# Optimization experiments

Hardware: AMD Instinct MI355X
Metric: run time of the kernel (lower is better)

## Reference

```python
import jax, jax.numpy as jnp
import numpy as np
from jax import lax

# dims
B, S, NF, E = 128, 256, 32, 4
D, H = 256, 4
DI = 2 * D            # mLSTM inner (up-projection) dim
DHM, DHS = DI // H, D // H
K = 4                 # causal conv kernel size
FF = 352              # gated FFN dim (~4/3 * D, sLSTM block post-FFN)
NE, NP = 100, 6


def _ln(x, g, b, eps=1e-5):
    mu = x.mean(-1, keepdims=True)
    v = x.var(-1, keepdims=True)
    return (x - mu) / jnp.sqrt(v + eps) * g + b


def _cconv(x, w, b):
    # depthwise causal conv1d: x [B,S,C], w [K,C], b [C]
    k = w.shape[0]
    xp = jnp.pad(x, ((0, 0), (k - 1, 0), (0, 0)))
    y = lax.conv_general_dilated(xp, w[:, None, :], (1,), 'VALID',
                                 dimension_numbers=('NWC', 'WIO', 'NWC'),
                                 feature_group_count=x.shape[-1])
    return y + b


def _headnorm(x, g, b, eps=1e-6):
    # per-head group norm: normalize over last (head-dim) axis
    mu = x.mean(-1, keepdims=True)
    v = x.var(-1, keepdims=True)
    return (x - mu) / jnp.sqrt(v + eps) * g + b


def _forward(emb_esn, emb_prof, W_in, b_in,
             m_ln_g, m_ln_b, m_Wup, m_bup, m_convW, m_convb,
             m_Wq, m_bq, m_Wk, m_bk, m_Wv, m_bv,
             m_Wi, m_bi, m_Wf, m_bf, m_skip, m_ng, m_nb, m_Wdown, m_bdown,
             s_ln_g, s_ln_b, s_convW, s_convb,
             s_Wi, s_bi, s_Wf, s_bf, s_Wz, s_bz, s_Wo, s_bo,
             s_Ri, s_Rf, s_Rz, s_Ro, s_ng, s_nb,
             f_ln_g, f_ln_b, f_Wup, f_bup, f_Wdown, f_bdown,
             h_W1, h_b1, h_W2, h_b2,
             x_sens, x_esn, x_prof):
    Bx, Sx = x_sens.shape[0], x_sens.shape[1]
    ve = jnp.broadcast_to(emb_esn[x_esn][:, None, :], (Bx, Sx, E))
    vp = jnp.broadcast_to(emb_prof[x_prof][:, None, :], (Bx, Sx, E))
    x = jnp.concatenate([x_sens, ve, vp], -1) @ W_in + b_in  # [B,S,D]

    # ---------------- block 0: mLSTM (parallel stabilized matrix memory) ----
    xn = _ln(x, m_ln_g, m_ln_b)
    up = xn @ m_Wup + m_bup
    xm, zg = jnp.split(up, 2, axis=-1)              # [B,S,DI] each
    a = jax.nn.silu(_cconv(xm, m_convW, m_convb))   # causal conv + SiLU
    q = a @ m_Wq + m_bq
    k = a @ m_Wk + m_bk
    v = xm @ m_Wv + m_bv
    gin = jnp.concatenate([q, k, v], -1)            # [B,S,3*DI]
    ipre = (gin @ m_Wi + m_bi).transpose(0, 2, 1)   # [B,H,S]
    fpre = (gin @ m_Wf + m_bf).transpose(0, 2, 1)

    def heads(t, dh):
        return t.reshape(Bx, Sx, H, dh).transpose(0, 2, 1, 3)
    qh, kh, vh = heads(q, DHM), heads(k, DHM), heads(v, DHM)  # [B,H,S,dh]

    lfg = jax.nn.log_sigmoid(fpre)
    F = jnp.cumsum(lfg, -1)                         # [B,H,S]
    logD = F[:, :, :, None] - F[:, :, None, :] + ipre[:, :, None, :]
    mask = jnp.tril(jnp.ones((Sx, Sx), bool))
    logD = jnp.where(mask, logD, -jnp.inf)
    mstab = logD.max(-1, keepdims=True)             # [B,H,S,1]
    Dm = jnp.exp(logD - mstab)
    scores = jnp.einsum('bhtd,bhsd->bhts', qh, kh) / np.sqrt(DHM).astype(np.float32)
    C = scores * Dm
    nrm = jnp.maximum(jnp.abs(C.sum(-1, keepdims=True)), jnp.exp(-mstab))
    hh = jnp.einsum('bhts,bhsd->bhtd', C, vh) / nrm
    hn = _headnorm(hh, m_ng.reshape(1, H, 1, DHM), m_nb.reshape(1, H, 1, DHM))
    hn = hn.transpose(0, 2, 1, 3).reshape(Bx, Sx, DI)
    hn = hn + m_skip * a                            # learnable skip from conv branch
    x = x + (hn * jax.nn.silu(zg)) @ m_Wdown + m_bdown

    # ---------------- block 1: sLSTM (stabilized scalar recurrent scan) -----
    xn = _ln(x, s_ln_g, s_ln_b)
    ac = jax.nn.silu(_cconv(xn, s_convW, s_convb))
    to_t = lambda t: t.reshape(Bx, Sx, H, DHS).transpose(1, 0, 2, 3)  # [S,B,H,dh]
    it = to_t(ac @ s_Wi + s_bi)
    ft = to_t(ac @ s_Wf + s_bf)
    zt = to_t(xn @ s_Wz + s_bz)
    ot = to_t(xn @ s_Wo + s_bo)

    def step(carry, xs):
        h, c, n, m = carry
        i0, f0, z0, o0 = xs
        ip = i0 + jnp.einsum('bhd,hde->bhe', h, s_Ri)
        fp = f0 + jnp.einsum('bhd,hde->bhe', h, s_Rf)
        zp = jnp.tanh(z0 + jnp.einsum('bhd,hde->bhe', h, s_Rz))
        op = jax.nn.sigmoid(o0 + jnp.einsum('bhd,hde->bhe', h, s_Ro))
        mn = jnp.maximum(fp + m, ip)
        ig = jnp.exp(ip - mn)
        fg = jnp.exp(fp + m - mn)
        c = fg * c + ig * zp
        n = fg * n + ig
        h = op * c / n
        return (h, c, n, mn), h

    init = tuple(jnp.zeros((Bx, H, DHS), x.dtype) for _ in range(4))
    _, hs = lax.scan(step, init, (it, ft, zt, ot))  # hs [S,B,H,dh]
    hs = _headnorm(hs, s_ng.reshape(1, 1, H, DHS), s_nb.reshape(1, 1, H, DHS))
    x = x + hs.transpose(1, 0, 2, 3).reshape(Bx, Sx, D)

    # gated FFN (sLSTM block post-feedforward)
    xn = _ln(x, f_ln_g, f_ln_b)
    g_, u_ = jnp.split(xn @ f_Wup + f_bup, 2, axis=-1)
    x = x + (jax.nn.gelu(g_) * u_) @ f_Wdown + f_bdown

    last = x[:, -1, :]
    return jax.nn.relu(last @ h_W1 + h_b1) @ h_W2 + h_b2


def setup_inputs() -> dict:
    key = jax.random.key(0)
    ks = iter(jax.random.split(key, 64))
    nrm = lambda sh, s=0.02: jax.random.normal(next(ks), sh, jnp.float32) * s
    z = lambda sh: jnp.zeros(sh, jnp.float32)
    o = lambda sh: jnp.ones(sh, jnp.float32)
    return dict(
        x_sens=jax.random.normal(next(ks), (B, S, NF), jnp.float32),
        x_esn=jax.random.randint(next(ks), (B,), 0, NE, jnp.int32),
        x_prof=jax.random.randint(next(ks), (B,), 0, NP, jnp.int32),
        emb_esn=nrm((NE + 1, E)), emb_prof=nrm((NP + 1, E)),
        W_in=nrm((NF + 2 * E, D)), b_in=z((D,)),
        m_ln_g=o((D,)), m_ln_b=z((D,)),
        m_Wup=nrm((D, 2 * DI)), m_bup=z((2 * DI,)),
        m_convW=nrm((K, DI)), m_convb=z((DI,)),
        m_Wq=nrm((DI, DI)), m_bq=z((DI,)),
        m_Wk=nrm((DI, DI)), m_bk=z((DI,)),
        m_Wv=nrm((DI, DI)), m_bv=z((DI,)),
        m_Wi=nrm((3 * DI, H)), m_bi=z((H,)),
        m_Wf=nrm((3 * DI, H)), m_bf=o((H,)),
        m_skip=o((DI,)), m_ng=o((DI,)), m_nb=z((DI,)),
        m_Wdown=nrm((DI, D)), m_bdown=z((D,)),
        s_ln_g=o((D,)), s_ln_b=z((D,)),
        s_convW=nrm((K, D)), s_convb=z((D,)),
        s_Wi=nrm((D, D)), s_bi=z((D,)),
        s_Wf=nrm((D, D)), s_bf=o((D,)),
        s_Wz=nrm((D, D)), s_bz=z((D,)),
        s_Wo=nrm((D, D)), s_bo=z((D,)),
        s_Ri=nrm((H, DHS, DHS)), s_Rf=nrm((H, DHS, DHS)),
        s_Rz=nrm((H, DHS, DHS)), s_Ro=nrm((H, DHS, DHS)),
        s_ng=o((D,)), s_nb=z((D,)),
        f_ln_g=o((D,)), f_ln_b=z((D,)),
        f_Wup=nrm((D, 2 * FF)), f_bup=z((2 * FF,)),
        f_Wdown=nrm((FF, D)), f_bdown=z((D,)),
        h_W1=nrm((D, 64), 0.05), h_b1=z((64,)),
        h_W2=nrm((64, 3), 0.05), h_b2=z((3,)),
    )


def reference(emb_esn, emb_prof, W_in, b_in,
              m_ln_g, m_ln_b, m_Wup, m_bup, m_convW, m_convb,
              m_Wq, m_bq, m_Wk, m_bk, m_Wv, m_bv,
              m_Wi, m_bi, m_Wf, m_bf, m_skip, m_ng, m_nb, m_Wdown, m_bdown,
              s_ln_g, s_ln_b, s_convW, s_convb,
              s_Wi, s_bi, s_Wf, s_bf, s_Wz, s_bz, s_Wo, s_bo,
              s_Ri, s_Rf, s_Rz, s_Ro, s_ng, s_nb,
              f_ln_g, f_ln_b, f_Wup, f_bup, f_Wdown, f_bdown,
              h_W1, h_b1, h_W2, h_b2,
              x_sens, x_esn, x_prof):
    return _forward(emb_esn, emb_prof, W_in, b_in,
                    m_ln_g, m_ln_b, m_Wup, m_bup, m_convW, m_convb,
                    m_Wq, m_bq, m_Wk, m_bk, m_Wv, m_bv,
                    m_Wi, m_bi, m_Wf, m_bf, m_skip, m_ng, m_nb, m_Wdown, m_bdown,
                    s_ln_g, s_ln_b, s_convW, s_convb,
                    s_Wi, s_bi, s_Wf, s_bf, s_Wz, s_bz, s_Wo, s_bo,
                    s_Ri, s_Rf, s_Rz, s_Ro, s_ng, s_nb,
                    f_ln_g, f_ln_b, f_Wup, f_bup, f_Wdown, f_bdown,
                    h_W1, h_b1, h_W2, h_b2,
                    x_sens, x_esn, x_prof)
```

## Files before the change

kernel.cpp:

```cpp
#include <hip/hip_runtime.h>
#include <cstdint>
#include <cstddef>


using u16 = unsigned short;
using u32 = unsigned int;

typedef __attribute__((ext_vector_type(8))) short short8;
typedef __attribute__((ext_vector_type(8))) unsigned short ushort8v;
typedef __attribute__((ext_vector_type(4))) float float4v;

#define DEVINL __device__ __forceinline__

DEVINL float b2f(u16 u){ u32 x = ((u32)u) << 16; return __builtin_bit_cast(float, x); }
DEVINL u16 f2b(float f){
  u32 x = __builtin_bit_cast(u32, f);
  u32 r = x + 0x7FFFu + ((x >> 16) & 1u);
  return (u16)(r >> 16);
}
DEVINL float ldval(float x){ return x; }
DEVINL float ldval(u16 x){ return b2f(x); }
DEVINL void stval(float* p, float v){ *p = v; }
DEVINL void stval(u16* p, float v){ *p = f2b(v); }

DEVINL void lds_barrier(){
  asm volatile("s_waitcnt lgkmcnt(0)" ::: "memory");
  __builtin_amdgcn_sched_barrier(0);
  __builtin_amdgcn_s_barrier();
  __builtin_amdgcn_sched_barrier(0);
}

DEVINL void dpp_sum2(float a, float b, float& oa, float& ob){
  int xa, xb;
  xa = __builtin_amdgcn_update_dpp(0, __builtin_bit_cast(int, a), 0x111, 0xf, 0xf, true);
  xb = __builtin_amdgcn_update_dpp(0, __builtin_bit_cast(int, b), 0x111, 0xf, 0xf, true);
  a += __builtin_bit_cast(float, xa); b += __builtin_bit_cast(float, xb);
  xa = __builtin_amdgcn_update_dpp(0, __builtin_bit_cast(int, a), 0x112, 0xf, 0xf, true);
  xb = __builtin_amdgcn_update_dpp(0, __builtin_bit_cast(int, b), 0x112, 0xf, 0xf, true);
  a += __builtin_bit_cast(float, xa); b += __builtin_bit_cast(float, xb);
  xa = __builtin_amdgcn_update_dpp(0, __builtin_bit_cast(int, a), 0x114, 0xf, 0xf, true);
  xb = __builtin_amdgcn_update_dpp(0, __builtin_bit_cast(int, b), 0x114, 0xf, 0xf, true);
  a += __builtin_bit_cast(float, xa); b += __builtin_bit_cast(float, xb);
  xa = __builtin_amdgcn_update_dpp(0, __builtin_bit_cast(int, a), 0x118, 0xf, 0xf, true);
  xb = __builtin_amdgcn_update_dpp(0, __builtin_bit_cast(int, b), 0x118, 0xf, 0xf, true);
  a += __builtin_bit_cast(float, xa); b += __builtin_bit_cast(float, xb);
  xa = __builtin_amdgcn_update_dpp(0, __builtin_bit_cast(int, a), 0x142, 0xf, 0xf, true);
  xb = __builtin_amdgcn_update_dpp(0, __builtin_bit_cast(int, b), 0x142, 0xf, 0xf, true);
  a += __builtin_bit_cast(float, xa); b += __builtin_bit_cast(float, xb);
  xa = __builtin_amdgcn_update_dpp(0, __builtin_bit_cast(int, a), 0x143, 0xf, 0xf, true);
  xb = __builtin_amdgcn_update_dpp(0, __builtin_bit_cast(int, b), 0x143, 0xf, 0xf, true);
  a += __builtin_bit_cast(float, xa); b += __builtin_bit_cast(float, xb);
  oa = __builtin_bit_cast(float, __builtin_amdgcn_readlane(__builtin_bit_cast(int, a), 63));
  ob = __builtin_bit_cast(float, __builtin_amdgcn_readlane(__builtin_bit_cast(int, b), 63));
}

constexpr int IN_N = 56;
constexpr long long IN_SIZES[IN_N] = {
  1048576, 128, 128, 404, 28, 10240, 256, 256, 256,
  262144, 1024, 2048, 512,
  262144, 512, 262144, 512, 262144, 512,
  6144, 4, 6144, 4,
  512, 512, 512, 131072, 256,
  256, 256, 1024, 256,
  65536, 256, 65536, 256, 65536, 256, 65536, 256,
  16384, 16384, 16384, 16384,
  256, 256,
  256, 256, 180224, 704, 90112, 256,
  16384, 64, 192, 3 };

constexpr bool is_wt_input(int i){
  return i==9 || i==13 || i==15 || i==17 || i==26 || i==32 || i==34 || i==36
      || i==38 || i==48 || i==50;
}

struct CvOff { long long off[IN_N+1]; };
constexpr CvOff make_off(){
  CvOff o{};
  long long a = 0;
  for (int i = 0; i < IN_N; i++){
    o.off[i] = a;
    long long s = IN_SIZES[i];
    if (i == 1 || i == 2 || is_wt_input(i)) s = 0;
    a += s;
  }
  o.off[IN_N] = a;
  return o;
}
constexpr CvOff CVOFF = make_off();
constexpr long long CV_TOTAL = CVOFF.off[IN_N];

constexpr int WT_NW = 11;
constexpr int WTB_IN[WT_NW] = {9, 13, 15, 17, 26, 32, 34, 36, 38, 48, 50};
constexpr int WTB_K[WT_NW]  = {256,512,512,512,512,256,256,256,256,256,352};
constexpr int WTB_N[WT_NW]  = {1024,512,512,512,256,256,256,256,256,704,256};
constexpr long long WTO[WT_NW+1] = {0, 262144, 524288, 786432, 1048576, 1179648,
  1245184, 1310720, 1376256, 1441792, 1622016, 1712128};
constexpr long long WT_ELEMS = WTO[WT_NW];

constexpr long long alignup(long long x){ return ((x + 255) / 256) * 256; }
constexpr long long TOK = 32768;
constexpr long long OFF_FLAG = alignup(CV_TOTAL);
constexpr long long OFF_IP  = OFF_FLAG + 64;
constexpr long long OFF_FP  = OFF_IP  + 131072;
constexpr long long OFF_F   = OFF_FP  + 131072;
constexpr long long OFF_G   = OFF_F   + 131072;
constexpr long long OFF_M   = OFF_G   + 131072;
constexpr long long OFF_X   = OFF_M   + 131072;
constexpr long long OFF_XN  = OFF_X   + TOK*256;
constexpr long long OFF_UP  = OFF_XN  + TOK*128;
constexpr long long OFF_A   = OFF_UP  + TOK*512;
constexpr long long OFF_Q   = OFF_A   + TOK*256;
constexpr long long OFF_K   = OFF_Q   + TOK*256;
constexpr long long OFF_V   = OFF_K   + TOK*256;
constexpr long long OFF_WT  = OFF_V   + TOK*256;
constexpr long long WS_END  = OFF_WT  + WT_ELEMS/2 + 256;


__global__ void detect_kernel(const void* mlng, int* flag){
  if (threadIdx.x == 0){
    u32 u = *(const u32*)mlng;
    *flag = (u == 0x3F803F80u) ? 1 : 0;
  }
}

struct InPtrs { const void* p[IN_N]; };

__global__ __launch_bounds__(256) void convert_kernel(InPtrs ptrs, float* __restrict__ cv,
                                                      const int* __restrict__ flag){
  long long gid = (long long)blockIdx.x * 256 + threadIdx.x;
  if (gid >= CV_TOTAL) return;
  int seg = 0;
#pragma unroll
  for (int i = 1; i < IN_N; i++) seg += (gid >= CVOFF.off[i]) ? 1 : 0;
  long long local = gid - CVOFF.off[seg];
  float v;
  if (*flag) v = b2f(((const u16*)ptrs.p[seg])[local]);
  else       v = ((const float*)ptrs.p[seg])[local];
  cv[gid] = v;
}

__global__ __launch_bounds__(256) void wtrans_kernel(InPtrs ptrs, u16* __restrict__ WTb,
                                                     const int* __restrict__ flag){
  int wz = blockIdx.z;
  int K = WTB_K[wz], N = WTB_N[wz];
  int n0 = blockIdx.x * 32, k0 = blockIdx.y * 32;
  if (n0 >= N || k0 >= K) return;
  const void* W = ptrs.p[WTB_IN[wz]];
  u16* WT = WTb + WTO[wz];
  __shared__ u16 tile[32][34];
  int tx = threadIdx.x & 31, ty = threadIdx.x >> 5;
  bool bf = (*flag != 0);
#pragma unroll
  for (int i = 0; i < 4; i++){
    size_t src = (size_t)(k0 + ty + i*8)*N + n0 + tx;
    tile[ty + i*8][tx] = bf ? ((const u16*)W)[src] : f2b(((const float*)W)[src]);
  }
  __syncthreads();
#pragma unroll
  for (int i = 0; i < 4; i++)
    WT[(size_t)(n0 + ty + i*8)*K + k0 + tx] = tile[tx][ty + i*8];
}

__global__ __launch_bounds__(256) void cat_kernel(const float* __restrict__ xs,
    const int* __restrict__ xe, const int* __restrict__ xp,
    const float* __restrict__ ee, const float* __restrict__ ep,
    float* __restrict__ CAT){
  int gid = blockIdx.x * 256 + threadIdx.x;
  int c = gid % 40; int t = gid / 40; int b = t >> 8;
  float v;
  if (c < 32)      v = xs[(size_t)t*32 + c];
  else if (c < 36) v = ee[xe[b]*4 + (c - 32)];
  else             v = ep[xp[b]*4 + (c - 36)];
  CAT[(size_t)t*40 + c] = v;
}

template<typename TA, typename TC>
__global__ __launch_bounds__(256) void gemm_kernel(
    const TA* __restrict__ A, int lda,
    const float* __restrict__ Wm, const float* __restrict__ bias,
    TC* __restrict__ Cc, int ldc, const float* __restrict__ resid,
    int M, int N, int K)
{
  __shared__ float As[16][68];
  __shared__ float Bs[16][68];
  const int bm = blockIdx.y * 64, bn = blockIdx.x * 64;
  const int tid = threadIdx.x, tx = tid & 15, ty = tid >> 4;
  float acc[4][4] = {};
  for (int k0 = 0; k0 < K; k0 += 16){
#pragma unroll
    for (int i = 0; i < 4; i++){
      int idx = tid + i*256;
      int m = idx >> 4, kq = idx & 15;
      As[kq][m] = (k0 + kq < K) ? ldval(A[(size_t)(bm + m)*lda + k0 + kq]) : 0.f;
      int kk = idx >> 6, n = idx & 63;
      Bs[kk][n] = (k0 + kk < K) ? Wm[(size_t)(k0 + kk)*N + bn + n] : 0.f;
    }
    __syncthreads();
#pragma unroll
    for (int kq = 0; kq < 16; kq++){
      float av[4], bv[4];
#pragma unroll
      for (int i = 0; i < 4; i++) av[i] = As[kq][ty*4 + i];
#pragma unroll
      for (int j = 0; j < 4; j++) bv[j] = Bs[kq][tx*4 + j];
#pragma unroll
      for (int i = 0; i < 4; i++)
#pragma unroll
        for (int j = 0; j < 4; j++) acc[i][j] += av[i]*bv[j];
    }
    __syncthreads();
  }
#pragma unroll
  for (int i = 0; i < 4; i++){
    int m = bm + ty*4 + i;
#pragma unroll
    for (int j = 0; j < 4; j++){
      int n = bn + tx*4 + j;
      float v = acc[i][j] + bias[n];
      if (resid) v += resid[(size_t)m*ldc + n];
      stval(&Cc[(size_t)m*ldc + n], v);
    }
  }
}

template<typename TC>
__global__ __launch_bounds__(256) void gemm_mfma(
    const u16* __restrict__ A, int lda,
    const u16* __restrict__ WT,
    const float* __restrict__ bias,
    TC* __restrict__ Cc, int ldc, const float* __restrict__ resid,
    int N, int K)
{
  __shared__ alignas(16) u16 As[128*40];
  __shared__ alignas(16) u16 Bs[128*40];
  const int bm = blockIdx.y * 128, bn = blockIdx.x * 128;
  const int tid = threadIdx.x;
  const int w = tid >> 6, lane = tid & 63, lm = lane & 15, q = lane >> 4;
  const int wm = w >> 1, wn = w & 1;
  float4v acc[4][4] = {};
  for (int k0 = 0; k0 < K; k0 += 32){
    __syncthreads();
#pragma unroll
    for (int c = tid; c < 512; c += 256){
      int r = c >> 2, ch = c & 3;
      *(uint4*)&As[r*40 + ch*8] = *(const uint4*)&A[(size_t)(bm + r)*lda + k0 + ch*8];
      int n = bn + r;
      uint4 bv = {0u,0u,0u,0u};
      if (n < N) bv = *(const uint4*)&WT[(size_t)n*K + k0 + ch*8];
      *(uint4*)&Bs[r*40 + ch*8] = bv;
    }
    __syncthreads();
    short8 a[4], b[4];
#pragma unroll
    for (int i = 0; i < 4; i++)
      a[i] = *(const short8*)&As[(wm*64 + i*16 + lm)*40 + q*8];
#pragma unroll
    for (int j = 0; j < 4; j++)
      b[j] = *(const short8*)&Bs[(wn*64 + j*16 + lm)*40 + q*8];
#pragma unroll
    for (int i = 0; i < 4; i++)
#pragma unroll
      for (int j = 0; j < 4; j++)
        acc[i][j] = __builtin_amdgcn_mfma_f32_16x16x32_bf16(a[i], b[j], acc[i][j], 0, 0, 0);
  }
#pragma unroll
  for (int i = 0; i < 4; i++){
#pragma unroll
    for (int j = 0; j < 4; j++){
      int col = bn + wn*64 + j*16 + lm;
      if (col < N){
#pragma unroll
        for (int r = 0; r < 4; r++){
          int row = bm + wm*64 + i*16 + q*4 + r;
          float v = acc[i][j][r] + bias[col];
          if (resid) v += resid[(size_t)row*ldc + col];
          stval(&Cc[(size_t)row*ldc + col], v);
        }
      }
    }
  }
}

__global__ __launch_bounds__(256) void ln_kernel(const float* __restrict__ Xin,
    const float* __restrict__ g, const float* __restrict__ b,
    u16* __restrict__ out, float eps){
  int t = blockIdx.x*4 + (threadIdx.x >> 6);
  int e = threadIdx.x & 63;
  float4 v = *(const float4*)&Xin[(size_t)t*256 + e*4];
  float su = v.x + v.y + v.z + v.w;
#pragma unroll
  for (int o = 32; o > 0; o >>= 1) su += __shfl_xor(su, o, 64);
  float mu = su * (1.f/256.f);
  float d0 = v.x - mu, d1 = v.y - mu, d2 = v.z - mu, d3 = v.w - mu;
  float sq = d0*d0 + d1*d1 + d2*d2 + d3*d3;
#pragma unroll
  for (int o = 32; o > 0; o >>= 1) sq += __shfl_xor(sq, o, 64);
  float rstd = rsqrtf(sq * (1.f/256.f) + eps);
  float4 gv = *(const float4*)&g[e*4];
  float4 bv = *(const float4*)&b[e*4];
  ushort4 o4;
  o4.x = f2b(d0*rstd*gv.x + bv.x);
  o4.y = f2b(d1*rstd*gv.y + bv.y);
  o4.z = f2b(d2*rstd*gv.z + bv.z);
  o4.w = f2b(d3*rstd*gv.w + bv.w);
  *(ushort4*)&out[(size_t)t*256 + e*4] = o4;
}

__global__ __launch_bounds__(256) void conv_silu_kernel(const u16* __restrict__ Xc, int ldx, int C,
    const float* __restrict__ w, const float* __restrict__ bias, u16* __restrict__ Y){
  int nc = C >> 3;
  long long gid = (long long)blockIdx.x * 256 + threadIdx.x;
  int c8 = (int)(gid % nc) * 8; long long t = gid / nc;
  int s = (int)(t & 255);
  float acc[8];
#pragma unroll
  for (int i = 0; i < 8; i++) acc[i] = bias[c8 + i];
#pragma unroll
  for (int j = 0; j < 4; j++){
    int so = s - 3 + j;
    if (so >= 0){
      ushort8v xv = *(const ushort8v*)&Xc[(size_t)(t - 3 + j)*ldx + c8];
#pragma unroll
      for (int i = 0; i < 8; i++) acc[i] += b2f(xv[i]) * w[j*C + c8 + i];
    }
  }
  ushort8v o8;
#pragma unroll
  for (int i = 0; i < 8; i++) o8[i] = f2b(acc[i] / (1.f + __expf(-acc[i])));
  *(ushort8v*)&Y[(size_t)t*C + c8] = o8;
}

__global__ __launch_bounds__(256) void gates_kernel(
    const u16* __restrict__ Q, const u16* __restrict__ Kb, const u16* __restrict__ V,
    const float* __restrict__ Wi, const float* __restrict__ bi,
    const float* __restrict__ Wf, const float* __restrict__ bf,
    float* __restrict__ IP, float* __restrict__ FP){
  int t = blockIdx.x; int tid = threadIdx.x;
  int o = tid & 7, seg = tid >> 3;
  int b = t >> 8, s = t & 255;
  int g = o & 3;
  const float* Wg = (o >= 4) ? Wf : Wi;
  float part = 0.f;
#pragma unroll
  for (int i = 0; i < 6; i++){
    int k8 = seg*48 + i*8;
    const u16* src; int off;
    if (k8 < 512){ src = Q; off = k8; }
    else if (k8 < 1024){ src = Kb; off = k8 - 512; }
    else { src = V; off = k8 - 1024; }
    ushort8v gv = *(const ushort8v*)&src[(size_t)t*512 + off];
#pragma unroll
    for (int j = 0; j < 8; j++) part += b2f(gv[j]) * Wg[(k8 + j)*4 + g];
  }
  __shared__ float red[256];
  red[tid] = part; __syncthreads();
  if (tid < 8){
    float tot = 0.f;
    for (int ss = 0; ss < 32; ss++) tot += red[ss*8 + tid];
    int gg = tid & 3;
    if (tid < 4) IP[(b*4 + gg)*256 + s] = tot + bi[gg];
    else         FP[(b*4 + gg)*256 + s] = tot + bf[gg];
  }
}

__global__ __launch_bounds__(256) void fscan_kernel(const float* __restrict__ IP,
    const float* __restrict__ FP, float* __restrict__ Fo, float* __restrict__ Go,
    float* __restrict__ Mo){
  int bh = blockIdx.x; int s = threadIdx.x;
  int idx = bh*256 + s;
  __shared__ float buf[256];
  float fp = FP[idx];
  float lfg = fminf(fp, 0.f) - log1pf(expf(-fabsf(fp)));
  float v = lfg;
  buf[s] = v; __syncthreads();
  for (int off = 1; off < 256; off <<= 1){
    float tv = (s >= off) ? buf[s - off] : 0.f;
    __syncthreads();
    v += tv; buf[s] = v;
    __syncthreads();
  }
  float Fv = v;
  float g = IP[idx] - Fv;
  float mv = g;
  buf[s] = mv; __syncthreads();
  for (int off = 1; off < 256; off <<= 1){
    float tv = (s >= off) ? buf[s - off] : -3.0e38f;
    __syncthreads();
    mv = fmaxf(mv, tv); buf[s] = mv;
    __syncthreads();
  }
  Fo[idx] = Fv; Go[idx] = g; Mo[idx] = mv;
}

__global__ __launch_bounds__(256) void attn_kernel(
    const u16* __restrict__ Q, const u16* __restrict__ Kb, const u16* __restrict__ V,
    const float* __restrict__ G, const float* __restrict__ Mx, const float* __restrict__ F,
    const u16* __restrict__ Ab, const u16* __restrict__ UPb,
    const float* __restrict__ ng, const float* __restrict__ nb,
    const float* __restrict__ skip, u16* __restrict__ Yb)
{
  int bh = blockIdx.y, b = bh >> 2, h = bh & 3;
  int tt = blockIdx.x, t0 = tt * 64;
  int tid = threadIdx.x;
  int w = tid >> 6, lane = tid & 63, lm = lane & 15, q = lane >> 4;
  int gbase = bh * 256;

  __shared__ alignas(16) u16 Qs[64*136];
  __shared__ alignas(16) u16 Ks[64*136];
  __shared__ alignas(16) u16 Vt[128*72];
  __shared__ alignas(16) u16 Ps[64*72];
  __shared__ float rs[64];

#pragma unroll
  for (int c = tid; c < 1024; c += 256){
    int r = c >> 4, ch = c & 15;
    *(uint4*)&Qs[r*136 + ch*8] =
      *(const uint4*)&Q[((size_t)(b*256 + t0 + r))*512 + h*128 + ch*8];
  }
  if (tid < 64) rs[tid] = 0.f;

  float mrow[4];
#pragma unroll
  for (int r = 0; r < 4; r++) mrow[r] = Mx[gbase + t0 + w*16 + q*4 + r];

  float4v acc2[8] = {};
  const float scale = 0.08838834764831845f;

  for (int ss = 0; ss <= tt; ss++){
    int s0 = ss * 64;
    __syncthreads();
#pragma unroll
    for (int c = tid; c < 1024; c += 256){
      int r = c >> 4, ch = c & 15;
      *(uint4*)&Ks[r*136 + ch*8] =
        *(const uint4*)&Kb[((size_t)(b*256 + s0 + r))*512 + h*128 + ch*8];
    }
#pragma unroll
    for (int c = tid; c < 1024; c += 256){
      int sl = c & 63, db = c >> 6;
      ushort8v v = *(const ushort8v*)&V[((size_t)(b*256 + s0 + sl))*512 + h*128 + db*8];
#pragma unroll
      for (int j = 0; j < 8; j++) Vt[(db*8 + j)*72 + sl] = v[j];
    }
    __syncthreads();
    float4v sacc[4] = {};
#pragma unroll
    for (int k0 = 0; k0 < 128; k0 += 32){
      short8 a = *(const short8*)&Qs[(w*16 + lm)*136 + k0 + q*8];
#pragma unroll
      for (int j = 0; j < 4; j++){
        short8 bb = *(const short8*)&Ks[(j*16 + lm)*136 + k0 + q*8];
        sacc[j] = __builtin_amdgcn_mfma_f32_16x16x32_bf16(a, bb, sacc[j], 0, 0, 0);
      }
    }
    float rp[4] = {0.f, 0.f, 0.f, 0.f};
#pragma unroll
    for (int j = 0; j < 4; j++){
      int scol = s0 + j*16 + lm;
      float gq = G[gbase + scol];
#pragma unroll
      for (int r = 0; r < 4; r++){
        int trow = t0 + w*16 + q*4 + r;
        float cval = (scol <= trow) ? sacc[j][r]*scale*__expf(gq - mrow[r]) : 0.f;
        Ps[(w*16 + q*4 + r)*72 + j*16 + lm] = f2b(cval);
        rp[r] += cval;
      }
    }
#pragma unroll
    for (int r = 0; r < 4; r++){
#pragma unroll
      for (int m = 1; m < 16; m <<= 1) rp[r] += __shfl_xor(rp[r], m, 16);
      if (lm == 0) rs[w*16 + q*4 + r] += rp[r];
    }
#pragma unroll
    for (int k0 = 0; k0 < 64; k0 += 32){
      short8 a = *(const short8*)&Ps[(w*16 + lm)*72 + k0 + q*8];
#pragma unroll
      for (int jd = 0; jd < 8; jd++){
        short8 bb = *(const short8*)&Vt[(jd*16 + lm)*72 + k0 + q*8];
        acc2[jd] = __builtin_amdgcn_mfma_f32_16x16x32_bf16(a, bb, acc2[jd], 0, 0, 0);
      }
    }
  }
  __syncthreads();
#pragma unroll
  for (int r = 0; r < 4; r++){
    int rl = w*16 + q*4 + r;
    int t = t0 + rl;
    float Fv = F[gbase + t];
    float nrm = fmaxf(fabsf(rs[rl]), __expf(-(Fv + mrow[r])));
    float inv = 1.f / nrm;
    float vv[8];
    float su = 0.f;
#pragma unroll
    for (int jd = 0; jd < 8; jd++){ vv[jd] = acc2[jd][r]*inv; su += vv[jd]; }
#pragma unroll
    for (int m = 1; m < 16; m <<= 1) su += __shfl_xor(su, m, 16);
    float mu = su * (1.f/128.f);
    float sq = 0.f;
#pragma unroll
    for (int jd = 0; jd < 8; jd++){ vv[jd] -= mu; sq += vv[jd]*vv[jd]; }
#pragma unroll
    for (int m = 1; m < 16; m <<= 1) sq += __shfl_xor(sq, m, 16);
    float rstd = rsqrtf(sq * (1.f/128.f) + 1e-6f);
#pragma unroll
    for (int jd = 0; jd < 8; jd++){
      int c = h*128 + jd*16 + lm;
      float hv = vv[jd]*rstd*ng[c] + nb[c];
      float av = b2f(Ab[(size_t)t*512 + c]);
      float zg = b2f(UPb[(size_t)t*1024 + 512 + c]);
      float sz = zg / (1.f + __expf(-zg));
      Yb[(size_t)t*512 + c] = f2b((hv + skip[c]*av)*sz);
    }
  }
}

__global__ __launch_bounds__(320) void scan_kernel(
    const float* __restrict__ G1, const float* __restrict__ G2,
    const float* __restrict__ Ri, const float* __restrict__ Rf,
    const float* __restrict__ Rz, const float* __restrict__ Ro,
    const float* __restrict__ sng, const float* __restrict__ snb,
    float* __restrict__ Xr){
  int bh = blockIdx.x; int b = bh >> 2, h = bh & 3;
  int e = threadIdx.x & 63;
  int w = threadIdx.x >> 6;
  __shared__ float4 part[2][4][64];
  __shared__ float hbuf[2][64];
  size_t xrow = ((size_t)b*256)*256 + h*64 + e;

  if (w < 4){
    float r0[16], r1[16], r2[16], r3[16];
    const float* Rp0 = Ri + h*4096 + w*1024;
    const float* Rp1 = Rf + h*4096 + w*1024;
    const float* Rp2 = Rz + h*4096 + w*1024;
    const float* Rp3 = Ro + h*4096 + w*1024;
#pragma unroll
    for (int d = 0; d < 16; d++){
      r0[d] = Rp0[d*64 + e];
      r1[d] = Rp1[d*64 + e];
      r2[d] = Rp2[d*64 + e];
      r3[d] = Rp3[d*64 + e];
    }
    const float* Gp = (w < 2) ? G1 : G2;
    size_t grow = ((size_t)b*256)*512 + ((w & 1) ? 256 : 0) + h*64 + e;
    float hS = 0.f, cS = 0.f, nS = 0.f, mS = 0.f;
    float gv = Gp[grow];
    float gn = Gp[grow + 512];
    for (int s = 0; s < 256; s++){
      float gn2 = 0.f;
      if (s < 254) gn2 = Gp[grow + (size_t)(s + 2)*512];
      float ai0 = 0.f, ai1 = 0.f, af0 = 0.f, af1 = 0.f;
      float az0 = 0.f, az1 = 0.f, ao0 = 0.f, ao1 = 0.f;
#pragma unroll
      for (int k = 0; k < 16; k += 2){
        float h0 = __builtin_bit_cast(float,
            __builtin_amdgcn_readlane(__builtin_bit_cast(int, hS), w*16 + k));
        float h1 = __builtin_bit_cast(float,
            __builtin_amdgcn_readlane(__builtin_bit_cast(int, hS), w*16 + k + 1));
        ai0 += h0*r0[k]; ai1 += h1*r0[k+1];
        af0 += h0*r1[k]; af1 += h1*r1[k+1];
        az0 += h0*r2[k]; az1 += h1*r2[k+1];
        ao0 += h0*r3[k]; ao1 += h1*r3[k+1];
      }
      float4 p;
      p.x = ai0 + ai1; p.y = af0 + af1; p.z = az0 + az1; p.w = ao0 + ao1;
      if      (w == 0) p.x += gv;
      else if (w == 1) p.y += gv;
      else if (w == 2) p.z += gv;
      else             p.w += gv;
      part[s & 1][w][e] = p;
      lds_barrier();
      float4 q0 = part[s & 1][0][e];
      float4 q1 = part[s & 1][1][e];
      float4 q2 = part[s & 1][2][e];
      float4 q3 = part[s & 1][3][e];
      float ip = (q0.x + q1.x) + (q2.x + q3.x);
      float fp = (q0.y + q1.y) + (q2.y + q3.y);
      float zr = (q0.z + q1.z) + (q2.z + q3.z);
      float og = (q0.w + q1.w) + (q2.w + q3.w);
      float zp = 1.f - 2.f*__builtin_amdgcn_rcpf(__expf(2.f*zr) + 1.f);
      float op = __builtin_amdgcn_rcpf(1.f + __expf(-og));
      float mn = fmaxf(fp + mS, ip);
      float ig = __expf(ip - mn);
      float fg = __expf(fp + mS - mn);
      cS = fg*cS + ig*zp;
      nS = fg*nS + ig;
      mS = mn;
      hS = op * cS * __builtin_amdgcn_rcpf(nS);
      if (w == 1) hbuf[s & 1][e] = hS;
      gv = gn; gn = gn2;
    }
    lds_barrier();
  } else {
    float gw = sng[h*64 + e], bw = snb[h*64 + e];
    float xp = 0.f, xc = 0.f;
    for (int s = 0; s < 256; s++){
      xc = Xr[xrow + (size_t)s*256];
      lds_barrier();
      if (s > 0){
        float hv = hbuf[(s - 1) & 1][e];
        float su, sq;
        dpp_sum2(hv, hv*hv, su, sq);
        float mu = su * (1.f/64.f);
        float var = fmaxf(sq * (1.f/64.f) - mu*mu, 0.f);
        float nv = (hv - mu) * rsqrtf(var + 1e-6f) * gw + bw;
        Xr[xrow + (size_t)(s - 1)*256] = xp + nv;
      }
      xp = xc;
    }
    lds_barrier();
    float hv = hbuf[1][e];
    float su, sq;
    dpp_sum2(hv, hv*hv, su, sq);
    float mu = su * (1.f/64.f);
    float var = fmaxf(sq * (1.f/64.f) - mu*mu, 0.f);
    float nv = (hv - mu) * rsqrtf(var + 1e-6f) * gw + bw;
    Xr[xrow + (size_t)255*256] = xp + nv;
  }
}

__global__ __launch_bounds__(256) void ffn_act_kernel(const u16* __restrict__ GU,
                                                      u16* __restrict__ P){
  long long gid = (long long)blockIdx.x * 256 + threadIdx.x;
  int j8 = (int)(gid % 44) * 8; long long t = gid / 44;
  ushort8v gv = *(const ushort8v*)&GU[(size_t)t*704 + j8];
  ushort8v uv = *(const ushort8v*)&GU[(size_t)t*704 + 352 + j8];
  ushort8v o8;
#pragma unroll
  for (int i = 0; i < 8; i++){
    float g = b2f(gv[i]);
    float u = b2f(uv[i]);
    float inner = 0.7978845608028654f * (g + 0.044715f*g*g*g);
    float gel = 0.5f * g * (1.f + tanhf(inner));
    o8[i] = f2b(gel * u);
  }
  *(ushort8v*)&P[(size_t)t*352 + j8] = o8;
}

__global__ __launch_bounds__(64) void head_kernel(const float* __restrict__ X,
    const float* __restrict__ W1, const float* __restrict__ b1,
    const float* __restrict__ W2, const float* __restrict__ b2,
    void* out, const int* __restrict__ flag){
  int b = blockIdx.x, j = threadIdx.x;
  __shared__ float L[256];
  __shared__ float H1[64];
  for (int i = j; i < 256; i += 64) L[i] = X[((size_t)(b*256 + 255))*256 + i];
  __syncthreads();
  float acc = b1[j];
  for (int d = 0; d < 256; d++) acc += L[d] * W1[d*64 + j];
  H1[j] = fmaxf(acc, 0.f);
  __syncthreads();
  if (j < 3){
    float o = b2[j];
    for (int k2 = 0; k2 < 64; k2++) o += H1[k2] * W2[k2*3 + j];
    if (*flag) ((u16*)out)[b*3 + j] = f2b(o);
    else       ((float*)out)[b*3 + j] = o;
  }
}

extern "C" void kernel_launch(void* const* d_in, const int* in_sizes, int n_in,
                              void* d_out, int out_size, void* d_ws, size_t ws_size,
                              hipStream_t stream)
{
  if (n_in != IN_N) return;
  for (int i = 0; i < IN_N; i++) if ((long long)in_sizes[i] != IN_SIZES[i]) return;
  if (ws_size < (size_t)WS_END * 4) return;
  if (out_size != 384) return;

  float* ws = (float*)d_ws;
  float* cv = ws;
  auto cvp = [&](int i){ return cv + CVOFF.off[i]; };

  int*   flag = (int*)(ws + OFF_FLAG);
  float* IP   = ws + OFF_IP;
  float* FP   = ws + OFF_FP;
  float* Fb   = ws + OFF_F;
  float* Gb   = ws + OFF_G;
  float* Mb   = ws + OFF_M;
  float* X    = ws + OFF_X;
  u16*   XNb  = (u16*)(ws + OFF_XN);
  u16*   UPb  = (u16*)(ws + OFF_UP);
  u16*   Ab   = (u16*)(ws + OFF_A);
  u16*   Qb   = (u16*)(ws + OFF_Q);
  u16*   Kbb  = (u16*)(ws + OFF_K);
  u16*   Vb   = (u16*)(ws + OFF_V);
  u16*   WTb  = (u16*)(ws + OFF_WT);
  float* CAT = ws + OFF_V;
  u16*   Yb  = Qb;
  u16*   ACb = Ab;
  float* G1f = ws + OFF_K;
  float* G2f = ws + OFF_UP;
  u16*   GUb = UPb;
  u16*   Pb  = Ab;

  auto wt = [&](int widx){ return WTb + WTO[widx]; };

  InPtrs ptrs;
  for (int i = 0; i < IN_N; i++) ptrs.p[i] = d_in[i];

  const int M = 32768;
  detect_kernel<<<1, 64, 0, stream>>>(d_in[7], flag);
  int cvblocks = (int)((CV_TOTAL + 255) / 256);
  convert_kernel<<<cvblocks, 256, 0, stream>>>(ptrs, cv, flag);
  wtrans_kernel<<<dim3(32, 16, 11), 256, 0, stream>>>(ptrs, WTb, flag);
  cat_kernel<<<5120, 256, 0, stream>>>(cvp(0), (const int*)d_in[1], (const int*)d_in[2],
                                       cvp(3), cvp(4), CAT);
  gemm_kernel<float, float><<<dim3(4, 512), 256, 0, stream>>>(CAT, 40, cvp(5), cvp(6),
      X, 256, nullptr, M, 256, 40);
  ln_kernel<<<8192, 256, 0, stream>>>(X, cvp(7), cvp(8), XNb, 1e-5f);
  gemm_mfma<u16><<<dim3(8, 256), 256, 0, stream>>>(XNb, 256, wt(0), cvp(10),
      UPb, 1024, nullptr, 1024, 256);
  conv_silu_kernel<<<8192, 256, 0, stream>>>(UPb, 1024, 512, cvp(11), cvp(12), Ab);
  gemm_mfma<u16><<<dim3(4, 256), 256, 0, stream>>>(Ab, 512, wt(1), cvp(14),
      Qb, 512, nullptr, 512, 512);
  gemm_mfma<u16><<<dim3(4, 256), 256, 0, stream>>>(Ab, 512, wt(2), cvp(16),
      Kbb, 512, nullptr, 512, 512);
  gemm_mfma<u16><<<dim3(4, 256), 256, 0, stream>>>(UPb, 1024, wt(3), cvp(18),
      Vb, 512, nullptr, 512, 512);
  gates_kernel<<<M, 256, 0, stream>>>(Qb, Kbb, Vb, cvp(19), cvp(20), cvp(21), cvp(22), IP, FP);
  fscan_kernel<<<512, 256, 0, stream>>>(IP, FP, Fb, Gb, Mb);
  attn_kernel<<<dim3(4, 512), 256, 0, stream>>>(Qb, Kbb, Vb, Gb, Mb, Fb,
      Ab, UPb, cvp(24), cvp(25), cvp(23), Yb);
  gemm_mfma<float><<<dim3(2, 256), 256, 0, stream>>>(Yb, 512, wt(4), cvp(27),
      X, 256, X, 256, 512);
  ln_kernel<<<8192, 256, 0, stream>>>(X, cvp(28), cvp(29), XNb, 1e-5f);
  conv_silu_kernel<<<4096, 256, 0, stream>>>(XNb, 256, 256, cvp(30), cvp(31), ACb);
  gemm_mfma<float><<<dim3(4, 256), 256, 0, stream>>>(ACb, 256, wt(5), cvp(33),
      G1f, 512, nullptr, 512, 256);
  gemm_mfma<float><<<dim3(4, 256), 256, 0, stream>>>(XNb, 256, wt(7), cvp(37),
      G2f, 512, nullptr, 512, 256);
  scan_kernel<<<512, 320, 0, stream>>>(G1f, G2f, cvp(40), cvp(41), cvp(42), cvp(43),
      cvp(44), cvp(45), X);
  ln_kernel<<<8192, 256, 0, stream>>>(X, cvp(46), cvp(47), XNb, 1e-5f);
  gemm_mfma<u16><<<dim3(6, 256), 256, 0, stream>>>(XNb, 256, wt(9), cvp(49),
      GUb, 704, nullptr, 704, 256);
  ffn_act_kernel<<<5632, 256, 0, stream>>>(GUb, Pb);
  gemm_mfma<float><<<dim3(2, 256), 256, 0, stream>>>(Pb, 352, wt(10), cvp(51),
      X, 256, X, 256, 352);
  head_kernel<<<128, 64, 0, stream>>>(X, cvp(52), cvp(53), cvp(54), cvp(55), d_out, flag);
}
```

Baseline: 1.152 ms.

## Double-buffer MFMA GEMM shared tiles and use plain syncthreads in sLSTM loop

The MFMA GEMM now uses two LDS buffers: the next K-slice's global loads are issued into registers before the current slice's MFMAs and written to the other buffer afterwards, so each iteration needs one barrier instead of two and global latency overlaps compute. Separately, the custom lds_barrier (lgkmcnt wait plus sched_barrier fences) in the sLSTM recurrence is replaced by __syncthreads. This doubles LDS use per block, which can lower occupancy. The barrier swap gives the compiler more scheduling freedom but may add waits on global memory traffic.

```diff
diff --git a/kernel.cpp b/kernel.cpp
--- a/kernel.cpp
+++ b/kernel.cpp
@@ -22,13 +22,6 @@
 DEVINL float ldval(u16 x){ return b2f(x); }
 DEVINL void stval(float* p, float v){ *p = v; }
 DEVINL void stval(u16* p, float v){ *p = f2b(v); }
-
-DEVINL void lds_barrier(){
-  asm volatile("s_waitcnt lgkmcnt(0)" ::: "memory");
-  __builtin_amdgcn_sched_barrier(0);
-  __builtin_amdgcn_s_barrier();
-  __builtin_amdgcn_sched_barrier(0);
-}
 
 DEVINL void dpp_sum2(float a, float b, float& oa, float& ob){
   int xa, xb;
@@ -231,32 +224,64 @@
     TC* __restrict__ Cc, int ldc, const float* __restrict__ resid,
     int N, int K)
 {
-  __shared__ alignas(16) u16 As[128*40];
-  __shared__ alignas(16) u16 Bs[128*40];
+  __shared__ alignas(16) u16 As[2][128*40];
+  __shared__ alignas(16) u16 Bs[2][128*40];
   const int bm = blockIdx.y * 128, bn = blockIdx.x * 128;
   const int tid = threadIdx.x;
   const int w = tid >> 6, lane = tid & 63, lm = lane & 15, q = lane >> 4;
   const int wm = w >> 1, wn = w & 1;
+  const int r0c = tid >> 2, ch0 = tid & 3;
+  const int r1c = (tid + 256) >> 2, ch1 = tid & 3;
   float4v acc[4][4] = {};
-  for (int k0 = 0; k0 < K; k0 += 32){
-    __syncthreads();
-#pragma unroll
-    for (int c = tid; c < 512; c += 256){
-      int r = c >> 2, ch = c & 3;
-      *(uint4*)&As[r*40 + ch*8] = *(const uint4*)&A[(size_t)(bm + r)*lda + k0 + ch*8];
-      int n = bn + r;
-      uint4 bv = {0u,0u,0u,0u};
-      if (n < N) bv = *(const uint4*)&WT[(size_t)n*K + k0 + ch*8];
-      *(uint4*)&Bs[r*40 + ch*8] = bv;
-    }
-    __syncthreads();
+
+  {
+    *(uint4*)&As[0][r0c*40 + ch0*8] = *(const uint4*)&A[(size_t)(bm + r0c)*lda + ch0*8];
+    int n0 = bn + r0c;
+    uint4 bv0 = {0u,0u,0u,0u};
+    if (n0 < N) bv0 = *(const uint4*)&WT[(size_t)n0*K + ch0*8];
+    *(uint4*)&Bs[0][r0c*40 + ch0*8] = bv0;
+    *(uint4*)&As[0][r1c*40 + ch1*8] = *(const uint4*)&A[(size_t)(bm + r1c)*lda + ch1*8];
+    int n1 = bn + r1c;
+    uint4 bv1 = {0u,0u,0u,0u};
+    if (n1 < N) bv1 = *(const uint4*)&WT[(size_t)n1*K + ch1*8];
+    *(uint4*)&Bs[0][r1c*40 + ch1*8] = bv1;
+  }
+  __syncthreads();
+  int cur = 0;
+  for (int k0 = 32; k0 < K; k0 += 32){
+    uint4 av0 = *(const uint4*)&A[(size_t)(bm + r0c)*lda + k0 + ch0*8];
+    uint4 av1 = *(const uint4*)&A[(size_t)(bm + r1c)*lda + k0 + ch1*8];
+    int n0 = bn + r0c, n1 = bn + r1c;
+    uint4 bv0 = {0u,0u,0u,0u}, bv1 = {0u,0u,0u,0u};
+    if (n0 < N) bv0 = *(const uint4*)&WT[(size_t)n0*K + k0 + ch0*8];
+    if (n1 < N) bv1 = *(const uint4*)&WT[(size_t)n1*K + k0 + ch1*8];
     short8 a[4], b[4];
 #pragma unroll
     for (int i = 0; i < 4; i++)
-      a[i] = *(const short8*)&As[(wm*64 + i*16 + lm)*40 + q*8];
+      a[i] = *(const short8*)&As[cur][(wm*64 + i*16 + lm)*40 + q*8];
 #pragma unroll
     for (int j = 0; j < 4; j++)
-      b[j] = *(const short8*)&Bs[(wn*64 + j*16 + lm)*40 + q*8];
+      b[j] = *(const short8*)&Bs[cur][(wn*64 + j*16 + lm)*40 + q*8];
+#pragma unroll
+    for (int i = 0; i < 4; i++)
+#pragma unroll
+      for (int j = 0; j < 4; j++)
+        acc[i][j] = __builtin_amdgcn_mfma_f32_16x16x32_bf16(a[i], b[j], acc[i][j], 0, 0, 0);
+    *(uint4*)&As[cur^1][r0c*40 + ch0*8] = av0;
+    *(uint4*)&Bs[cur^1][r0c*40 + ch0*8] = bv0;
+    *(uint4*)&As[cur^1][r1c*40 + ch1*8] = av1;
+    *(uint4*)&Bs[cur^1][r1c*40 + ch1*8] = bv1;
+    __syncthreads();
+    cur ^= 1;
+  }
+  {
+    short8 a[4], b[4];
+#pragma unroll
+    for (int i = 0; i < 4; i++)
+      a[i] = *(const short8*)&As[cur][(wm*64 + i*16 + lm)*40 + q*8];
+#pragma unroll
+    for (int j = 0; j < 4; j++)
+      b[j] = *(const short8*)&Bs[cur][(wn*64 + j*16 + lm)*40 + q*8];
 #pragma unroll
     for (int i = 0; i < 4; i++)
 #pragma unroll
@@ -569,7 +594,7 @@
       else if (w == 2) p.z += gv;
       else             p.w += gv;
       part[s & 1][w][e] = p;
-      lds_barrier();
+      __syncthreads();
       float4 q0 = part[s & 1][0][e];
       float4 q1 = part[s & 1][1][e];
       float4 q2 = part[s & 1][2][e];
@@ -590,13 +615,13 @@
       if (w == 1) hbuf[s & 1][e] = hS;
       gv = gn; gn = gn2;
     }
-    lds_barrier();
+    __syncthreads();
   } else {
     float gw = sng[h*64 + e], bw = snb[h*64 + e];
     float xp = 0.f, xc = 0.f;
     for (int s = 0; s < 256; s++){
       xc = Xr[xrow + (size_t)s*256];
-      lds_barrier();
+      __syncthreads();
       if (s > 0){
         float hv = hbuf[(s - 1) & 1][e];
         float su, sq;
@@ -608,7 +633,7 @@
       }
       xp = xc;
     }
-    lds_barrier();
+    __syncthreads();
     float hv = hbuf[1][e];
     float su, sq;
     dpp_sum2(hv, hv*hv, su, sq);
```

Result: faster. 1.063 ms (-7.7%).
